# Optimization experiments

Hardware: AMD Instinct MI355X
Metric: run time of the kernel (lower is better)

## Reference

```python
import jax, jax.numpy as jnp
import numpy as np

B, T, C, H = 4, 2048, 1024, 16
HD = C // H


def setup_inputs() -> dict:
    key = jax.random.key(0)
    k1, k2, k3 = jax.random.split(key, 3)
    x = jax.random.normal(k1, (B, T, C), dtype=jnp.float32)
    w_attn = jax.random.normal(k2, (C, 3 * C), dtype=jnp.float32) * (1.0 / np.sqrt(C))
    b_attn = jnp.zeros((3 * C,), dtype=jnp.float32)
    w_proj = jax.random.normal(k3, (C, C), dtype=jnp.float32) * (1.0 / np.sqrt(C))
    b_proj = jnp.zeros((C,), dtype=jnp.float32)
    return {"x": x, "w_attn": w_attn, "b_attn": b_attn, "w_proj": w_proj, "b_proj": b_proj}


def reference(x, w_attn, b_attn, w_proj, b_proj):
    # QKV projection: [B,T,3C]
    qkv = x @ w_attn + b_attn
    q, k, v = jnp.split(qkv, 3, axis=-1)
    # [B,H,T,HD]
    q = q.reshape(B, T, H, HD).swapaxes(1, 2)
    k = k.reshape(B, T, H, HD).swapaxes(1, 2)
    v = v.reshape(B, T, H, HD).swapaxes(1, 2)
    scale = 1.0 / jnp.sqrt(jnp.float32(HD))
    attn = jnp.einsum('bhqd,bhkd->bhqk', q, k) * scale  # [B,H,T,T]
    causal = jnp.tril(jnp.ones((T, T), dtype=bool))
    attn = jnp.where(causal[None, None, :, :], attn, -jnp.inf)
    attn = jax.nn.softmax(attn, axis=-1)
    y = jnp.einsum('bhqk,bhkd->bhqd', attn, v)  # [B,H,T,HD]
    y = y.swapaxes(1, 2).reshape(B, T, C)
    return y @ w_proj + b_proj
```

## Files before the change

kernel.cpp:

```cpp
#include <hip/hip_runtime.h>
#include <hip/hip_bf16.h>

#define BB 4
#define TT 2048
#define CC 1024
#define HH 16
#define HD 64
#define NQ (3*CC)
#define QSCALE 0.18033688011112042f

typedef __attribute__((ext_vector_type(8))) short bf16x8;
typedef __attribute__((ext_vector_type(4))) short short4_t;
typedef __attribute__((ext_vector_type(4))) float f32x4;

#define MFMA(a,b,c) __builtin_amdgcn_mfma_f32_16x16x32_bf16(a,b,c,0,0,0)

#define ASYNC16(gsrc, ldst) \
  __builtin_amdgcn_global_load_lds((const __attribute__((address_space(1))) void*)(gsrc), \
                                   (__attribute__((address_space(3))) void*)(ldst), 16, 0, 0)

#define SWZA(row) (((((row) & 7) + (((row) >> 3) & 3)) & 7) << 3)

static __device__ __forceinline__ short f2bf(float f){
    union { float f; unsigned u; } v; v.f = f;
    unsigned r = v.u + 0x7FFFu + ((v.u >> 16) & 1u);
    return (short)(r >> 16);
}
static __device__ __forceinline__ unsigned cvtpk(float a, float b){
    unsigned r;
    asm("v_cvt_pk_bf16_f32 %0, %1, %2" : "=v"(r) : "v"(a), "v"(b));
    return r;
}

__global__ __launch_bounds__(256)
void convert_x(const float* __restrict__ x, short* __restrict__ xb)
{
    int i = (blockIdx.x * 256 + threadIdx.x) * 8;
    float4 a = *reinterpret_cast<const float4*>(&x[i]);
    float4 b = *reinterpret_cast<const float4*>(&x[i+4]);
    bf16x8 o = { f2bf(a.x), f2bf(a.y), f2bf(a.z), f2bf(a.w),
                 f2bf(b.x), f2bf(b.y), f2bf(b.z), f2bf(b.w) };
    *reinterpret_cast<bf16x8*>(&xb[i]) = o;
}

__global__ __launch_bounds__(256)
void transpose_w(const float* __restrict__ w, short* __restrict__ wT, int N)
{
    __shared__ short sm[64*72];
    const int kt0 = blockIdx.x * 64;
    const int nt0 = blockIdx.y * 64;
    const int t = threadIdx.x;
    const int r  = t >> 4;
    const int c4 = (t & 15) * 4;
#pragma unroll
    for (int it = 0; it < 4; it++){
        int k = r + it*16;
        float4 v = *reinterpret_cast<const float4*>(&w[(size_t)(kt0 + k)*N + nt0 + c4]);
        sm[(c4+0)*72 + k] = f2bf(v.x);
        sm[(c4+1)*72 + k] = f2bf(v.y);
        sm[(c4+2)*72 + k] = f2bf(v.z);
        sm[(c4+3)*72 + k] = f2bf(v.w);
    }
    __syncthreads();
    const int nl = t >> 2;
    const int kc = (t & 3) * 16;
    bf16x8 o0 = *reinterpret_cast<const bf16x8*>(&sm[nl*72 + kc]);
    bf16x8 o1 = *reinterpret_cast<const bf16x8*>(&sm[nl*72 + kc + 8]);
    short* dst = &wT[(size_t)(nt0 + nl)*CC + kt0 + kc];
    *reinterpret_cast<bf16x8*>(dst)     = o0;
    *reinterpret_cast<bf16x8*>(dst + 8) = o1;
}

__global__ __launch_bounds__(256, 2)
void qkv_gemm(const short* __restrict__ xb, const short* __restrict__ wT,
              const float* __restrict__ bias,
              short* __restrict__ qb, short* __restrict__ kb, short* __restrict__ vtb)
{
    __shared__ short smem[128*136];
    short* As = smem;
    short* Bs = smem + 8192;
    const int bid = blockIdx.x;
    const int swz = (bid & 7) * 192 + (bid >> 3);
    const int bm = swz / (NQ/128);
    const int bn = swz % (NQ/128);
    const int m0 = bm*128, n0 = bn*128;
    const int t  = threadIdx.x;
    const int wid = t >> 6, lane = t & 63;
    const int wr = wid >> 1, wc = wid & 1;
    const int l15 = lane & 15, lh = lane >> 4;

    f32x4 acc[4][4];
#pragma unroll
    for (int i=0;i<4;i++)
#pragma unroll
      for (int j=0;j<4;j++) acc[i][j] = (f32x4)0.f;

    for (int k0 = 0; k0 < CC; k0 += 64) {
        __syncthreads();
#pragma unroll
        for (int i=0;i<4;i++){
            int u   = (wid*4 + i)*64 + lane;
            int row = u >> 3, c = u & 7;
            int cs  = c ^ (row & 7);
            ASYNC16(&xb[(size_t)(m0+row)*CC + k0 + cs*8], &As[(wid*4+i)*512]);
            ASYNC16(&wT[(size_t)(n0+row)*CC + k0 + cs*8], &Bs[(wid*4+i)*512]);
        }
        __syncthreads();
#pragma unroll
        for (int ks=0;ks<2;ks++){
            bf16x8 a[4], b[4];
#pragma unroll
            for (int m=0;m<4;m++){
                int row = wr*64 + m*16 + l15;
                a[m] = *reinterpret_cast<const bf16x8*>(&As[row*64 + (((ks<<2)|lh) ^ (row&7))*8]);
            }
#pragma unroll
            for (int n=0;n<4;n++){
                int col = wc*64 + n*16 + l15;
                b[n] = *reinterpret_cast<const bf16x8*>(&Bs[col*64 + (((ks<<2)|lh) ^ (col&7))*8]);
            }
#pragma unroll
            for (int m=0;m<4;m++)
#pragma unroll
              for (int n=0;n<4;n++)
                acc[m][n] = MFMA(a[m], b[n], acc[m][n]);
        }
    }

    if (n0 < 2*CC) {
#pragma unroll
        for (int n=0;n<4;n++){
            int col = n0 + wc*64 + n*16 + l15;
            int sect = col >> 10;
            int cc = col & 1023;
            int h = cc >> 6, d = cc & 63;
            float bv = bias[col];
            short* dst = (sect==0) ? qb : kb;
            float mul = (sect==0) ? QSCALE : 1.f;
#pragma unroll
            for (int m=0;m<4;m++)
#pragma unroll
              for (int r=0;r<4;r++){
                int row = m0 + wr*64 + m*16 + lh*4 + r;
                int b_ = row >> 11, tt_ = row & (TT-1);
                float v = (acc[m][n][r] + bv) * mul;
                dst[((size_t)(b_*HH + h)*TT + tt_)*HD + d] = f2bf(v);
              }
        }
    } else {
        __syncthreads();
        short* Ts = smem;
#pragma unroll
        for (int n=0;n<4;n++){
            int colL = wc*64 + n*16 + l15;
            float bv = bias[n0 + colL];
#pragma unroll
            for (int m=0;m<4;m++){
                int rowL = wr*64 + m*16 + lh*4;
                short4_t pk = { f2bf(acc[m][n][0]+bv), f2bf(acc[m][n][1]+bv),
                                f2bf(acc[m][n][2]+bv), f2bf(acc[m][n][3]+bv) };
                *reinterpret_cast<short4_t*>(&Ts[colL*136 + rowL]) = pk;
            }
        }
        __syncthreads();
        const int b_ = m0 >> 11, t0 = m0 & (TT-1);
        const int cc0 = n0 - 2*CC;
#pragma unroll
        for (int pass=0;pass<2;pass++){
            int c = (t >> 2) + pass*64;
            int vcol = cc0 + c;
            short* dst = vtb + ((size_t)(b_*HH + (vcol>>6))*HD + (vcol&63))*TT + t0;
#pragma unroll
            for (int it=0;it<4;it++){
                int r0 = (t & 3)*8 + it*32;
                *reinterpret_cast<bf16x8*>(&dst[r0]) =
                    *reinterpret_cast<const bf16x8*>(&Ts[c*136 + r0]);
            }
        }
    }
}

__global__ __launch_bounds__(256, 3)
void attn_kernel(const short* __restrict__ qb, const short* __restrict__ kb,
                 const short* __restrict__ vtb, short* __restrict__ yb)
{
    __shared__ short Ks[2][64*64];
    __shared__ short Vt[2][64*64];
    __shared__ short Ps[4][32*64];

    const int bh = blockIdx.x;
    const int qt = 15 - blockIdx.y;
    const int b_ = bh >> 4, h = bh & 15;
    const short* qp  = qb  + (size_t)bh*TT*HD;
    const short* kp  = kb  + (size_t)bh*TT*HD;
    const short* vtp = vtb + (size_t)bh*HD*TT;
    const int t = threadIdx.x, wid = t >> 6, lane = t & 63;
    const int l15 = lane & 15, lh = lane >> 4;

    int kvoffB[8];
#pragma unroll
    for (int ks=0;ks<2;ks++)
#pragma unroll
      for (int i=0;i<4;i++){
        int row = i*16 + l15;
        kvoffB[ks*4+i] = ((row*64 + ks*32 + lh*8) ^ SWZA(row)) * 2;
      }
    int pwB[8];
#pragma unroll
    for (int m=0;m<2;m++){
        int qloc = m*16 + l15;
#pragma unroll
        for (int f=0;f<4;f++)
            pwB[m*4+f] = ((qloc*64 + f*16 + lh*4) ^ SWZA(qloc)) * 2;
    }
    char* KsB = (char*)&Ks[0][0];
    char* VtB = (char*)&Vt[0][0];
    char* PsB = (char*)&Ps[wid][0];

    const int su0 = (wid*2+0)*64 + lane;
    const int su1 = (wid*2+1)*64 + lane;
    const int sr0 = su0 >> 3, sc0 = (su0 & 7) ^ (SWZA(su0 >> 3) >> 3);
    const int sr1 = su1 >> 3, sc1 = (su1 & 7) ^ (SWZA(su1 >> 3) >> 3);

    const short* kg0 = kp  + (size_t)sr0*HD + sc0*8;
    const short* kg1 = kp  + (size_t)sr1*HD + sc1*8;
    const short* vg0 = vtp + (size_t)sr0*TT + sc0*8;
    const short* vg1 = vtp + (size_t)sr1*TT + sc1*8;

    const bf16x8 ones = { 0x3F80,0x3F80,0x3F80,0x3F80,0x3F80,0x3F80,0x3F80,0x3F80 };

    auto stageN = [&](int buf){
        ASYNC16(kg0, &Ks[buf][(wid*2+0)*512]);
        ASYNC16(kg1, &Ks[buf][(wid*2+1)*512]);
        ASYNC16(vg0, &Vt[buf][(wid*2+0)*512]);
        ASYNC16(vg1, &Vt[buf][(wid*2+1)*512]);
        kg0 += 64*HD; kg1 += 64*HD; vg0 += 64; vg1 += 64;
    };

    const int wq0 = qt*128 + wid*32;

    bf16x8 qf[2][2];
#pragma unroll
    for (int m=0;m<2;m++)
#pragma unroll
      for (int ks=0;ks<2;ks++)
        qf[m][ks] = *reinterpret_cast<const bf16x8*>(
            &qp[(size_t)(wq0 + m*16 + l15)*HD + ks*32 + lh*8]);

    f32x4 po[2][4];
    f32x4 pden[2];
#pragma unroll
    for (int m=0;m<2;m++){
        pden[m] = (f32x4)0.f;
#pragma unroll
        for (int n=0;n<4;n++) po[m][n] = (f32x4)0.f;
    }

    const int ntk = 2*(qt + 1);

    stageN(0);
    __syncthreads();

    for (int kt = 0; kt < ntk; ){
#pragma unroll
        for (int cur = 0; cur < 2; cur++, kt++){
            const int kv0 = kt*64;
            if (kt+1 < ntk) stageN(cur ^ 1);

            if (kv0 <= wq0 + 31){
                f32x4 s[2][4];
#pragma unroll
                for (int m=0;m<2;m++)
#pragma unroll
                  for (int f=0;f<4;f++) s[m][f] = (f32x4)0.f;
                __builtin_amdgcn_s_setprio(1);
#pragma unroll
                for (int ks=0;ks<2;ks++){
#pragma unroll
                    for (int f=0;f<4;f++){
                        bf16x8 kf = *reinterpret_cast<const bf16x8*>(
                            KsB + cur*8192 + kvoffB[ks*4+f]);
                        s[0][f] = MFMA(kf, qf[0][ks], s[0][f]);
                        s[1][f] = MFMA(kf, qf[1][ks], s[1][f]);
                    }
                }
                __builtin_amdgcn_s_setprio(0);
#pragma unroll
                for (int m=0;m<2;m++){
                    if (kv0 + 63 > wq0 + m*16){
                        int qm = wq0 + m*16 + l15;
#pragma unroll
                        for (int f=0;f<4;f++)
#pragma unroll
                          for (int r=0;r<4;r++){
                            int kv = kv0 + f*16 + lh*4 + r;
                            if (kv > qm) s[m][f][r] = -1e30f;
                          }
                    }
                }
#pragma unroll
                for (int m=0;m<2;m++){
#pragma unroll
                    for (int f=0;f<4;f++){
                        uint2 pk;
                        pk.x = cvtpk(exp2f(s[m][f][0]), exp2f(s[m][f][1]));
                        pk.y = cvtpk(exp2f(s[m][f][2]), exp2f(s[m][f][3]));
                        *reinterpret_cast<uint2*>(PsB + pwB[m*4+f]) = pk;
                    }
                }
                __builtin_amdgcn_s_setprio(1);
#pragma unroll
                for (int k2=0;k2<2;k2++){
                    bf16x8 pa[2];
#pragma unroll
                    for (int m=0;m<2;m++)
                        pa[m] = *reinterpret_cast<const bf16x8*>(PsB + kvoffB[k2*4+m]);
                    pden[0] = MFMA(pa[0], ones, pden[0]);
                    pden[1] = MFMA(pa[1], ones, pden[1]);
#pragma unroll
                    for (int n=0;n<4;n++){
                        bf16x8 vf = *reinterpret_cast<const bf16x8*>(
                            VtB + cur*8192 + kvoffB[k2*4+n]);
                        po[0][n] = MFMA(pa[0], vf, po[0][n]);
                        po[1][n] = MFMA(pa[1], vf, po[1][n]);
                    }
                }
                __builtin_amdgcn_s_setprio(0);
            }

            __syncthreads();
        }
    }

#pragma unroll
    for (int m=0;m<2;m++){
        float rcp[4];
#pragma unroll
        for (int r=0;r<4;r++) rcp[r] = 1.f / pden[m][r];
#pragma unroll
        for (int n=0;n<4;n++)
#pragma unroll
          for (int r=0;r<4;r++){
            int q = wq0 + m*16 + lh*4 + r;
            int dd = n*16 + l15;
            yb[(size_t)(b_*TT + q)*CC + h*HD + dd] = f2bf(po[m][n][r] * rcp[r]);
          }
    }
}

__global__ __launch_bounds__(256, 2)
void proj_gemm(const short* __restrict__ y, const short* __restrict__ wpT,
               const float* __restrict__ bias, float* __restrict__ out)
{
    __shared__ short As[128*64];
    __shared__ short Bs[128*64];
    const int bid = blockIdx.x;
    const int swz = (bid & 7) * 64 + (bid >> 3);
    const int bm = swz >> 3, bn = swz & 7;
    const int m0 = bm*128, n0 = bn*128;
    const int t  = threadIdx.x;
    const int wid = t >> 6, lane = t & 63;
    const int wr = wid >> 1, wc = wid & 1;
    const int l15 = lane & 15, lh = lane >> 4;

    f32x4 acc[4][4];
#pragma unroll
    for (int i=0;i<4;i++)
#pragma unroll
      for (int j=0;j<4;j++) acc[i][j] = (f32x4)0.f;

    for (int k0 = 0; k0 < CC; k0 += 64) {
        __syncthreads();
#pragma unroll
        for (int i=0;i<4;i++){
            int u   = (wid*4 + i)*64 + lane;
            int row = u >> 3, c = u & 7;
            int cs  = c ^ (row & 7);
            ASYNC16(&y[(size_t)(m0+row)*CC + k0 + cs*8],   &As[(wid*4+i)*512]);
            ASYNC16(&wpT[(size_t)(n0+row)*CC + k0 + cs*8], &Bs[(wid*4+i)*512]);
        }
        __syncthreads();
#pragma unroll
        for (int ks=0;ks<2;ks++){
            bf16x8 a[4], b[4];
#pragma unroll
            for (int m=0;m<4;m++){
                int row = wr*64 + m*16 + l15;
                a[m] = *reinterpret_cast<const bf16x8*>(&As[row*64 + (((ks<<2)|lh) ^ (row&7))*8]);
            }
#pragma unroll
            for (int n=0;n<4;n++){
                int col = wc*64 + n*16 + l15;
                b[n] = *reinterpret_cast<const bf16x8*>(&Bs[col*64 + (((ks<<2)|lh) ^ (col&7))*8]);
            }
#pragma unroll
            for (int m=0;m<4;m++)
#pragma unroll
              for (int n=0;n<4;n++)
                acc[m][n] = MFMA(a[m], b[n], acc[m][n]);
        }
    }

#pragma unroll
    for (int n=0;n<4;n++){
        int col = n0 + wc*64 + n*16 + l15;
        float bv = bias[col];
#pragma unroll
        for (int m=0;m<4;m++)
#pragma unroll
          for (int r=0;r<4;r++){
            int row = m0 + wr*64 + m*16 + lh*4 + r;
            out[(size_t)row*CC + col] = acc[m][n][r] + bv;
          }
    }
}

extern "C" void kernel_launch(void* const* d_in, const int* in_sizes, int n_in,
                              void* d_out, int out_size, void* d_ws, size_t ws_size,
                              hipStream_t stream) {
    const float* x      = (const float*)d_in[0];
    const float* w_attn = (const float*)d_in[1];
    const float* b_attn = (const float*)d_in[2];
    const float* w_proj = (const float*)d_in[3];
    const float* b_proj = (const float*)d_in[4];
    float* out = (float*)d_out;

    const size_t S = (size_t)BB*TT*CC;
    short* qb  = (short*)d_ws;
    short* kb  = qb + S;
    short* vtb = kb + S;
    short* yx  = vtb + S;
    short* wT  = yx + S;
    short* wpT = wT + (size_t)NQ*CC;

    convert_x<<<dim3(S/(256*8)), 256, 0, stream>>>(x, yx);
    transpose_w<<<dim3(CC/64, NQ/64), 256, 0, stream>>>(w_attn, wT, NQ);
    transpose_w<<<dim3(CC/64, CC/64), 256, 0, stream>>>(w_proj, wpT, CC);
    qkv_gemm<<<dim3((BB*TT/128)*(NQ/128)), 256, 0, stream>>>(yx, wT, b_attn, qb, kb, vtb);
    attn_kernel<<<dim3(BB*HH, TT/128), 256, 0, stream>>>(qb, kb, vtb, yx);
    proj_gemm<<<dim3((BB*TT/128)*(CC/128)), 256, 0, stream>>>(yx, wpT, b_proj, out);
}
```

Baseline: 170.9 us.

## Rewrite QKV GEMM with 256x256 tiles, 512 threads and 4-stage async LDS ring

The QKV projection GEMM moves from 128x128 tiles with 256 threads and a single-buffered LDS stage to 256x256 tiles with 512 threads (8 waves, each holding 128x64 of output). The K loop now steps 32 at a time through a 4-deep ring of async global-to-LDS loads, synchronised with explicit vmcnt waits and barriers, and raises wave priority around the MFMA blocks. The aim is to hide load latency and cut global traffic per FLOP through larger-tile reuse. In exchange it uses 128KB of LDS and larger accumulators, which limits occupancy, and it launches only 384 blocks. The V-transpose epilogue is done in two halves through the same LDS.

```diff
diff --git a/kernel.cpp b/kernel.cpp
--- a/kernel.cpp
+++ b/kernel.cpp
@@ -71,61 +71,91 @@
     *reinterpret_cast<bf16x8*>(dst + 8) = o1;
 }
 
-__global__ __launch_bounds__(256, 2)
+
+#define QKV_STAGE(s) do{                                                     \
+    short* ab_ = ring + (s)*8192;                                            \
+    ASYNC16(pA0, ab_ + ldsW0); ASYNC16(pA1, ab_ + ldsW1);                    \
+    short* bb_ = ring + 32768 + (s)*8192;                                    \
+    ASYNC16(pB0, bb_ + ldsW0); ASYNC16(pB1, bb_ + ldsW1);                    \
+    pA0 += 32; pA1 += 32; pB0 += 32; pB1 += 32; }while(0)
+
+#define QKV_COMPUTE(s) do{                                                   \
+    const short* base_ = ring + (s)*8192;                                    \
+    bf16x8 a_[8], b_[4];                                                     \
+    _Pragma("unroll") for(int m_=0;m_<8;m_++)                                \
+        a_[m_] = *reinterpret_cast<const bf16x8*>(base_ + aOff[m_]);         \
+    _Pragma("unroll") for(int n_=0;n_<4;n_++)                                \
+        b_[n_] = *reinterpret_cast<const bf16x8*>(base_ + bOff[n_]);         \
+    __builtin_amdgcn_s_setprio(1);                                           \
+    _Pragma("unroll") for(int m_=0;m_<8;m_++)                                \
+      _Pragma("unroll") for(int n_=0;n_<4;n_++)                              \
+        acc[m_][n_] = MFMA(a_[m_], b_[n_], acc[m_][n_]);                     \
+    __builtin_amdgcn_s_setprio(0); }while(0)
+
+#define QKV_SYNC(N) do{                                                      \
+    asm volatile("s_waitcnt vmcnt(" #N ")" ::: "memory");                    \
+    __builtin_amdgcn_s_barrier();                                            \
+    __builtin_amdgcn_sched_barrier(0); }while(0)
+
+__global__ __launch_bounds__(512, 2)
 void qkv_gemm(const short* __restrict__ xb, const short* __restrict__ wT,
               const float* __restrict__ bias,
               short* __restrict__ qb, short* __restrict__ kb, short* __restrict__ vtb)
 {
-    __shared__ short smem[128*136];
-    short* As = smem;
-    short* Bs = smem + 8192;
+    __shared__ short ring[65536];
     const int bid = blockIdx.x;
-    const int swz = (bid & 7) * 192 + (bid >> 3);
-    const int bm = swz / (NQ/128);
-    const int bn = swz % (NQ/128);
-    const int m0 = bm*128, n0 = bn*128;
+    const int swz = (bid & 7) * 48 + (bid >> 3);
+    const int bm = swz / 12, bn = swz % 12;
+    const int m0 = bm*256, n0 = bn*256;
     const int t  = threadIdx.x;
     const int wid = t >> 6, lane = t & 63;
-    const int wr = wid >> 1, wc = wid & 1;
+    const int wr = wid >> 2, wc = wid & 3;
     const int l15 = lane & 15, lh = lane >> 4;
 
-    f32x4 acc[4][4];
-#pragma unroll
-    for (int i=0;i<4;i++)
-#pragma unroll
-      for (int j=0;j<4;j++) acc[i][j] = (f32x4)0.f;
-
-    for (int k0 = 0; k0 < CC; k0 += 64) {
-        __syncthreads();
-#pragma unroll
-        for (int i=0;i<4;i++){
-            int u   = (wid*4 + i)*64 + lane;
-            int row = u >> 3, c = u & 7;
-            int cs  = c ^ (row & 7);
-            ASYNC16(&xb[(size_t)(m0+row)*CC + k0 + cs*8], &As[(wid*4+i)*512]);
-            ASYNC16(&wT[(size_t)(n0+row)*CC + k0 + cs*8], &Bs[(wid*4+i)*512]);
-        }
-        __syncthreads();
-#pragma unroll
-        for (int ks=0;ks<2;ks++){
-            bf16x8 a[4], b[4];
-#pragma unroll
-            for (int m=0;m<4;m++){
-                int row = wr*64 + m*16 + l15;
-                a[m] = *reinterpret_cast<const bf16x8*>(&As[row*64 + (((ks<<2)|lh) ^ (row&7))*8]);
-            }
-#pragma unroll
-            for (int n=0;n<4;n++){
-                int col = wc*64 + n*16 + l15;
-                b[n] = *reinterpret_cast<const bf16x8*>(&Bs[col*64 + (((ks<<2)|lh) ^ (col&7))*8]);
-            }
-#pragma unroll
-            for (int m=0;m<4;m++)
-#pragma unroll
-              for (int n=0;n<4;n++)
-                acc[m][n] = MFMA(a[m], b[n], acc[m][n]);
-        }
-    }
+    int srow0, scol0, srow1, scol1;
+    { int u = t;        srow0 = u >> 2; int c = u & 3; scol0 = c ^ ((srow0 >> 1) & 3); }
+    { int u = 512 + t;  srow1 = u >> 2; int c = u & 3; scol1 = c ^ ((srow1 >> 1) & 3); }
+    const short* pA0 = xb + (size_t)(m0+srow0)*CC + scol0*8;
+    const short* pA1 = xb + (size_t)(m0+srow1)*CC + scol1*8;
+    const short* pB0 = wT + (size_t)(n0+srow0)*CC + scol0*8;
+    const short* pB1 = wT + (size_t)(n0+srow1)*CC + scol1*8;
+    const int ldsW0 = wid*512;
+    const int ldsW1 = 4096 + wid*512;
+
+    int aOff[8], bOff[4];
+#pragma unroll
+    for (int m=0;m<8;m++){
+        int row = wr*128 + m*16 + l15;
+        aOff[m] = row*32 + (lh ^ ((row>>1)&3))*8;
+    }
+#pragma unroll
+    for (int n=0;n<4;n++){
+        int row = wc*64 + n*16 + l15;
+        bOff[n] = 32768 + row*32 + (lh ^ ((row>>1)&3))*8;
+    }
+
+    f32x4 acc[8][4];
+#pragma unroll
+    for (int m=0;m<8;m++)
+#pragma unroll
+      for (int n=0;n<4;n++) acc[m][n] = (f32x4)0.f;
+
+    QKV_STAGE(0); QKV_STAGE(1); QKV_STAGE(2);
+    QKV_SYNC(8);
+
+    for (int blk = 0; blk < 7; blk++){
+#pragma unroll
+        for (int j = 0; j < 4; j++){
+            QKV_STAGE((j+3)&3);
+            QKV_COMPUTE(j);
+            QKV_SYNC(8);
+        }
+    }
+    QKV_STAGE(3); QKV_COMPUTE(0); QKV_SYNC(8);
+    QKV_COMPUTE(1);               QKV_SYNC(4);
+    QKV_COMPUTE(2);               QKV_SYNC(0);
+    QKV_COMPUTE(3);
+    __syncthreads();
 
     if (n0 < 2*CC) {
 #pragma unroll
@@ -138,44 +168,46 @@
             short* dst = (sect==0) ? qb : kb;
             float mul = (sect==0) ? QSCALE : 1.f;
 #pragma unroll
-            for (int m=0;m<4;m++)
+            for (int m=0;m<8;m++)
 #pragma unroll
               for (int r=0;r<4;r++){
-                int row = m0 + wr*64 + m*16 + lh*4 + r;
+                int row = m0 + wr*128 + m*16 + lh*4 + r;
                 int b_ = row >> 11, tt_ = row & (TT-1);
                 float v = (acc[m][n][r] + bv) * mul;
                 dst[((size_t)(b_*HH + h)*TT + tt_)*HD + d] = f2bf(v);
               }
         }
     } else {
-        __syncthreads();
-        short* Ts = smem;
-#pragma unroll
-        for (int n=0;n<4;n++){
-            int colL = wc*64 + n*16 + l15;
-            float bv = bias[n0 + colL];
-#pragma unroll
-            for (int m=0;m<4;m++){
-                int rowL = wr*64 + m*16 + lh*4;
-                short4_t pk = { f2bf(acc[m][n][0]+bv), f2bf(acc[m][n][1]+bv),
-                                f2bf(acc[m][n][2]+bv), f2bf(acc[m][n][3]+bv) };
-                *reinterpret_cast<short4_t*>(&Ts[colL*136 + rowL]) = pk;
+        const int b_ = m0 >> 11, t0 = m0 & (TT-1);
+#pragma unroll
+        for (int hh=0; hh<2; hh++){
+            if ((wc >> 1) == hh){
+#pragma unroll
+                for (int n=0;n<4;n++){
+                    int colL = (wc&1)*64 + n*16 + l15;
+                    float bv = bias[n0 + hh*128 + colL];
+#pragma unroll
+                    for (int m=0;m<8;m++){
+                        int rowL = wr*128 + m*16 + lh*4;
+                        short4_t pk = { f2bf(acc[m][n][0]+bv), f2bf(acc[m][n][1]+bv),
+                                        f2bf(acc[m][n][2]+bv), f2bf(acc[m][n][3]+bv) };
+                        *reinterpret_cast<short4_t*>(&ring[colL*264 + rowL]) = pk;
+                    }
+                }
             }
-        }
-        __syncthreads();
-        const int b_ = m0 >> 11, t0 = m0 & (TT-1);
-        const int cc0 = n0 - 2*CC;
-#pragma unroll
-        for (int pass=0;pass<2;pass++){
-            int c = (t >> 2) + pass*64;
-            int vcol = cc0 + c;
-            short* dst = vtb + ((size_t)(b_*HH + (vcol>>6))*HD + (vcol&63))*TT + t0;
-#pragma unroll
-            for (int it=0;it<4;it++){
-                int r0 = (t & 3)*8 + it*32;
-                *reinterpret_cast<bf16x8*>(&dst[r0]) =
-                    *reinterpret_cast<const bf16x8*>(&Ts[c*136 + r0]);
+            __syncthreads();
+            {
+                int c = t >> 2;
+                int vcol = n0 - 2*CC + hh*128 + c;
+                short* dst = vtb + ((size_t)(b_*HH + (vcol>>6))*HD + (vcol&63))*TT + t0;
+#pragma unroll
+                for (int it=0; it<8; it++){
+                    int r0 = (t&3)*8 + it*32;
+                    *reinterpret_cast<bf16x8*>(&dst[r0]) =
+                        *reinterpret_cast<const bf16x8*>(&ring[c*264 + r0]);
+                }
             }
+            __syncthreads();
         }
     }
 }
@@ -436,7 +468,7 @@
     convert_x<<<dim3(S/(256*8)), 256, 0, stream>>>(x, yx);
     transpose_w<<<dim3(CC/64, NQ/64), 256, 0, stream>>>(w_attn, wT, NQ);
     transpose_w<<<dim3(CC/64, CC/64), 256, 0, stream>>>(w_proj, wpT, CC);
-    qkv_gemm<<<dim3((BB*TT/128)*(NQ/128)), 256, 0, stream>>>(yx, wT, b_attn, qb, kb, vtb);
+    qkv_gemm<<<dim3(384), 512, 0, stream>>>(yx, wT, b_attn, qb, kb, vtb);
     attn_kernel<<<dim3(BB*HH, TT/128), 256, 0, stream>>>(qb, kb, vtb, yx);
     proj_gemm<<<dim3((BB*TT/128)*(CC/128)), 256, 0, stream>>>(yx, wpT, b_proj, out);
 }
```

Result: no change. 174.1 us (+1.9%).
